# Optimization experiments

Hardware: AMD Instinct MI355X
Metric: run time of the kernel (lower is better)

Reference implementation:

```python
import jax, jax.numpy as jnp
import numpy as np
from jax.scipy.special import logsumexp

G, E, K, D, B, L, M, KN = 32000, 256, 8, 6, 4, 512, 64, 4
STEP, EPS = 0.05, 1.0


def setup_inputs() -> dict:
    key = jax.random.key(0)
    ks = jax.random.split(key, 16)
    s = 0.05  # weight scale for numerical stability
    return {
        'masked': jax.random.randint(ks[0], (B, L), 0, G),
        'unmasked': jax.random.randint(ks[1], (B, L), 0, G),
        'mask': jax.random.randint(ks[2], (B, M), 0, L),
        'summer': jnp.ones((B, M), jnp.float32),
        'embed': jax.random.normal(ks[3], (G, E), jnp.float32) * s,
        'pos': jax.random.normal(ks[4], (L, E), jnp.float32) * s,
        'Wt': jax.random.normal(ks[5], (D, E, E), jnp.float32) * s,
        'Wc': jax.random.normal(ks[6], (D, E, E), jnp.float32) * s,
        'Wq': jax.random.normal(ks[7], (D, K * E, E), jnp.float32) * s,
        'Wd': jax.random.normal(ks[8], (D, K * E, K * E), jnp.float32) * s,
        'Wo': jax.random.normal(ks[9], (D, K * E, E), jnp.float32) * s,
        'Wkc': jax.random.normal(ks[10], (E * KN, E), jnp.float32) * s,
        'bkc': jax.random.normal(ks[11], (E * KN,), jnp.float32) * s,
        'Wem': jax.random.normal(ks[12], (E, E), jnp.float32) * s,
    }


def _norm(x):
    # y / (eps + y.std(-1, unbiased)); torch std is ddof=1
    return x / (EPS + jnp.std(x, axis=-1, ddof=1, keepdims=True))


def reference(masked, unmasked, mask, summer, embed, pos, Wt, Wc, Wq, Wd, Wo, Wkc, bkc, Wem):
    b, l = masked.shape
    # batch init: token + positional embedding, normalized
    xsa = _norm(embed[masked] + pos[None, :l])  # (B,L,E)
    inv_sqrt_e = 1.0 / (E ** 0.5)
    for d in range(D):
        # local transition terms (roll +/- 1 along sequence)
        xsad = jax.nn.relu(jnp.roll(xsa, 1, axis=1) @ Wt[d]) @ Wc[d]
        xsad = xsad + jax.nn.relu(jnp.roll(xsa, -1, axis=1) @ Wc[d].T) @ Wt[d].T
        # QKV_Attention: K query heads against raw xsa keys/values
        q = (xsa @ Wq[d].T).reshape(b, l, K, E)           # (B,L,K,E)
        hijk = jnp.einsum('blke,bme->blkm', q, xsa) * inv_sqrt_e  # (B,L,K,L)
        pijk = jax.nn.softmax(hijk, axis=-1)
        yik = jnp.einsum('blkm,bme->blke', pijk, xsa)      # (B,L,K,E)
        xid = yik.reshape(b, l, K * E)
        # Dense -> ReLU -> Dense (mode 1)
        xidact = jax.nn.relu(xid @ Wd[d].T)                # (B,L,K*E)
        xsad = xsad + xidact @ Wo[d]                       # (B,L,E)
        # gradnorm + residual update + layernorm
        xsad = _norm(xsad)
        xsa = _norm(xsa + STEP * xsad)
    # loss head: gather masked positions
    lptok = jnp.take_along_axis(xsa, mask[:, :, None], axis=1)  # (B,M,E)
    m = mask.shape[1]
    xx = (lptok @ Wkc.T + bkc).reshape(b, m * KN, E)       # kchoice
    xx = jnp.einsum('bne,ble->bnl', xx, xsa)               # (B,M*KN,L)
    xx = jnp.einsum('bnl,ble->bne', xx, xsa)               # (B,M*KN,E)
    logits = (xx @ Wem) @ embed.T                          # (B,M*KN,G)
    k_lp = jax.nn.log_softmax(logits, axis=-1).reshape(b, m, KN, G)
    lp = logsumexp(k_lp, axis=-2) - jnp.float32(np.log(KN))  # (B,M,G)
    tgt = jnp.take_along_axis(unmasked, mask, axis=1)       # (B,M)
    cent = jnp.take_along_axis(lp, tgt[:, :, None], axis=-1)[:, :, 0]
    loss = -(cent * summer).sum(-1) / jnp.clip(summer.sum(-1), 1.0, None)
    return loss
```

## Files before the change

### kernel.cpp

```cpp
#include <hip/hip_runtime.h>
#include <math.h>
#include <stdint.h>

#define G_ 32000
#define E_ 256
#define K_ 8
#define D_ 6
#define B_ 4
#define L_ 512
#define M_ 64
#define KN_ 4
#define STEP_ 0.05f
#define BL_ (B_ * L_)
#define KE_ (K_ * E_)
#define NSPLIT_ 50
#define GCH_ 10

typedef __attribute__((ext_vector_type(8))) short short8;
typedef __attribute__((ext_vector_type(4))) float f32x4;
typedef __attribute__((ext_vector_type(4))) short short4v;

__device__ __forceinline__ short f2bf(float f) {
  unsigned u = __builtin_bit_cast(unsigned, f);
  unsigned r = (u + 0x7fffu + ((u >> 16) & 1u)) >> 16;
  return (short)r;
}
__device__ __forceinline__ float bf2f(short h) {
  return __builtin_bit_cast(float, ((unsigned)(unsigned short)h) << 16);
}

__device__ __forceinline__ void gload16(const void* g, void* l) {
  __builtin_amdgcn_global_load_lds(
      reinterpret_cast<const __attribute__((address_space(1))) void*>(
          reinterpret_cast<uintptr_t>(g)),
      reinterpret_cast<__attribute__((address_space(3))) void*>(
          reinterpret_cast<uintptr_t>(l)),
      16, 0, 0);
}

__device__ __forceinline__ float wsum(float v) {
#pragma unroll
  for (int o = 32; o > 0; o >>= 1) v += __shfl_xor(v, o, 64);
  return v;
}
__device__ __forceinline__ float block_sum(float v, float* sm) {
  v = wsum(v);
  int wid = threadIdx.x >> 6, lane = threadIdx.x & 63;
  if (lane == 0) sm[wid] = v;
  __syncthreads();
  float r = sm[0] + sm[1] + sm[2] + sm[3];
  __syncthreads();
  return r;
}

template <bool RELU, bool OBF>
__global__ __launch_bounds__(256) void mg128x64_k(
    const short* __restrict__ A, const short* __restrict__ B,
    void* __restrict__ Cg, int Kd, int lda, int ldb, int ldc) {
  __shared__ short As[128 * 64];
  __shared__ short Bs[64 * 64];
  int m0 = blockIdx.y * 128, n0 = blockIdx.x * 64;
  int t = threadIdx.x, w = t >> 6, l = t & 63;
  int l16 = l & 15, qd = l >> 4, hi8 = qd * 8;
  int wr_ = w >> 1, wc_ = w & 1;
  int sr = l >> 3;
  int scol = ((l & 7) * 8) ^ (sr << 3);
  f32x4 acc[4][2];
#pragma unroll
  for (int i = 0; i < 4; i++)
#pragma unroll
    for (int j = 0; j < 2; j++) acc[i][j] = {0.f, 0.f, 0.f, 0.f};

  for (int k0 = 0; k0 < Kd; k0 += 64) {
    __syncthreads();
#pragma unroll
    for (int c = 0; c < 4; c++) {
      int sub = w * 4 + c;
      int r = sub * 8 + sr;
      gload16(A + (long)(m0 + r) * lda + k0 + scol, &As[sub * 512]);
    }
#pragma unroll
    for (int c = 0; c < 2; c++) {
      int sub = w * 2 + c;
      int r = sub * 8 + sr;
      gload16(B + (long)(n0 + r) * ldb + k0 + scol, &Bs[sub * 512]);
    }
    __syncthreads();
#pragma unroll
    for (int ks = 0; ks < 2; ks++) {
      short8 af[4], bf[2];
#pragma unroll
      for (int rf = 0; rf < 4; rf++) {
        int row = wr_ * 64 + rf * 16 + l16;
        af[rf] = *(const short8*)&As[(row * 64 + ks * 32 + hi8) ^ ((row & 7) << 3)];
      }
#pragma unroll
      for (int cf = 0; cf < 2; cf++) {
        int row = wc_ * 32 + cf * 16 + l16;
        bf[cf] = *(const short8*)&Bs[(row * 64 + ks * 32 + hi8) ^ ((row & 7) << 3)];
      }
#pragma unroll
      for (int rf = 0; rf < 4; rf++)
#pragma unroll
        for (int cf = 0; cf < 2; cf++)
          acc[rf][cf] = __builtin_amdgcn_mfma_f32_16x16x32_bf16(
              af[rf], bf[cf], acc[rf][cf], 0, 0, 0);
    }
  }
#pragma unroll
  for (int rf = 0; rf < 4; rf++) {
#pragma unroll
    for (int cf = 0; cf < 2; cf++) {
      int col = n0 + wc_ * 32 + cf * 16 + l16;
#pragma unroll
      for (int j = 0; j < 4; j++) {
        int row = m0 + wr_ * 64 + rf * 16 + qd * 4 + j;
        float v = acc[rf][cf][j];
        if (RELU) v = fmaxf(v, 0.f);
        long idx = (long)row * ldc + col;
        if (OBF) ((short*)Cg)[idx] = f2bf(v);
        else ((float*)Cg)[idx] = v;
      }
    }
  }
}

__global__ __launch_bounds__(256) void mg64sk_k(
    const short* __restrict__ A, const short* __restrict__ B,
    float* __restrict__ P, int Klen, int lda, int ldb, int ldc, long pstride) {
  __shared__ short As[64 * 64];
  __shared__ short Bs[64 * 64];
  int z = blockIdx.z;
  int kbase = z * Klen;
  int m0 = blockIdx.y * 64, n0 = blockIdx.x * 64;
  int t = threadIdx.x, w = t >> 6, l = t & 63;
  int l16 = l & 15, qd = l >> 4, hi8 = qd * 8;
  int wr_ = w >> 1, wc_ = w & 1;
  int sr = l >> 3;
  int scol = ((l & 7) * 8) ^ (sr << 3);
  f32x4 acc[2][2];
#pragma unroll
  for (int i = 0; i < 2; i++)
#pragma unroll
    for (int j = 0; j < 2; j++) acc[i][j] = {0.f, 0.f, 0.f, 0.f};

  for (int k0 = 0; k0 < Klen; k0 += 64) {
    __syncthreads();
#pragma unroll
    for (int c = 0; c < 2; c++) {
      int sub = w * 2 + c;
      int r = sub * 8 + sr;
      gload16(A + (long)(m0 + r) * lda + kbase + k0 + scol, &As[sub * 512]);
      gload16(B + (long)(n0 + r) * ldb + kbase + k0 + scol, &Bs[sub * 512]);
    }
    __syncthreads();
#pragma unroll
    for (int ks = 0; ks < 2; ks++) {
      short8 af[2], bf[2];
#pragma unroll
      for (int rf = 0; rf < 2; rf++) {
        int row = wr_ * 32 + rf * 16 + l16;
        af[rf] = *(const short8*)&As[(row * 64 + ks * 32 + hi8) ^ ((row & 7) << 3)];
      }
#pragma unroll
      for (int cf = 0; cf < 2; cf++) {
        int row = wc_ * 32 + cf * 16 + l16;
        bf[cf] = *(const short8*)&Bs[(row * 64 + ks * 32 + hi8) ^ ((row & 7) << 3)];
      }
#pragma unroll
      for (int rf = 0; rf < 2; rf++)
#pragma unroll
        for (int cf = 0; cf < 2; cf++)
          acc[rf][cf] = __builtin_amdgcn_mfma_f32_16x16x32_bf16(
              af[rf], bf[cf], acc[rf][cf], 0, 0, 0);
    }
  }
  float* Pz = P + z * pstride;
#pragma unroll
  for (int rf = 0; rf < 2; rf++) {
#pragma unroll
    for (int cf = 0; cf < 2; cf++) {
      int col = n0 + wc_ * 32 + cf * 16 + l16;
#pragma unroll
      for (int j = 0; j < 4; j++) {
        int row = m0 + wr_ * 32 + rf * 16 + qd * 4 + j;
        Pz[(long)row * ldc + col] = acc[rf][cf][j];
      }
    }
  }
}

template <bool BIAS>
__global__ __launch_bounds__(256) void mgh_k(
    const short* __restrict__ Ag, const short* __restrict__ Bg,
    short* __restrict__ Cg, const float* __restrict__ bias, int Kd, int lda,
    int ldb, int ldc, long sA, long sB, long sC) {
  __shared__ short As[64 * 64];
  __shared__ short Bs[64 * 64];
  int z = blockIdx.z;
  const short* A = Ag + z * sA;
  const short* B = Bg + z * sB;
  short* C = Cg + z * sC;
  int m0 = blockIdx.y * 64, n0 = blockIdx.x * 64;
  int t = threadIdx.x, w = t >> 6, l = t & 63;
  int l16 = l & 15, qd = l >> 4, hi8 = qd * 8;
  int wr_ = w >> 1, wc_ = w & 1;
  int sr = l >> 3;
  int scol = ((l & 7) * 8) ^ (sr << 3);
  f32x4 acc[2][2];
#pragma unroll
  for (int i = 0; i < 2; i++)
#pragma unroll
    for (int j = 0; j < 2; j++) acc[i][j] = {0.f, 0.f, 0.f, 0.f};

  for (int k0 = 0; k0 < Kd; k0 += 64) {
    __syncthreads();
#pragma unroll
    for (int c = 0; c < 2; c++) {
      int sub = w * 2 + c;
      int r = sub * 8 + sr;
      gload16(A + (long)(m0 + r) * lda + k0 + scol, &As[sub * 512]);
      gload16(B + (long)(n0 + r) * ldb + k0 + scol, &Bs[sub * 512]);
    }
    __syncthreads();
#pragma unroll
    for (int ks = 0; ks < 2; ks++) {
      short8 af[2], bf[2];
#pragma unroll
      for (int rf = 0; rf < 2; rf++) {
        int row = wr_ * 32 + rf * 16 + l16;
        af[rf] = *(const short8*)&As[(row * 64 + ks * 32 + hi8) ^ ((row & 7) << 3)];
      }
#pragma unroll
      for (int cf = 0; cf < 2; cf++) {
        int row = wc_ * 32 + cf * 16 + l16;
        bf[cf] = *(const short8*)&Bs[(row * 64 + ks * 32 + hi8) ^ ((row & 7) << 3)];
      }
#pragma unroll
      for (int rf = 0; rf < 2; rf++)
#pragma unroll
        for (int cf = 0; cf < 2; cf++)
          acc[rf][cf] = __builtin_amdgcn_mfma_f32_16x16x32_bf16(
              af[rf], bf[cf], acc[rf][cf], 0, 0, 0);
    }
  }
#pragma unroll
  for (int rf = 0; rf < 2; rf++) {
#pragma unroll
    for (int cf = 0; cf < 2; cf++) {
      int col = n0 + wc_ * 32 + cf * 16 + l16;
      float bv = BIAS ? bias[col] : 0.f;
#pragma unroll
      for (int j = 0; j < 4; j++) {
        int row = m0 + wr_ * 32 + rf * 16 + qd * 4 + j;
        C[(long)row * ldc + col] = f2bf(acc[rf][cf][j] + bv);
      }
    }
  }
}

__global__ __launch_bounds__(256) void tpair_k(
    const short* __restrict__ xsa_bf, const short* __restrict__ wtT,
    const short* __restrict__ wcb, short* __restrict__ T) {
  __shared__ short As[64 * 64];
  __shared__ short Bs[64 * 64];
  int z = blockIdx.z;
  const short* Bb = z ? wcb : wtT;
  int rollv = z ? -1 : 1;
  int m0 = blockIdx.y * 64, n0 = blockIdx.x * 64;
  int t = threadIdx.x, w = t >> 6, l = t & 63;
  int l16 = l & 15, qd = l >> 4, hi8 = qd * 8;
  int wr_ = w >> 1, wc_ = w & 1;
  int sr = l >> 3;
  int scol = ((l & 7) * 8) ^ (sr << 3);
  f32x4 acc[2][2];
#pragma unroll
  for (int i = 0; i < 2; i++)
#pragma unroll
    for (int j = 0; j < 2; j++) acc[i][j] = {0.f, 0.f, 0.f, 0.f};
  for (int k0 = 0; k0 < E_; k0 += 64) {
    __syncthreads();
#pragma unroll
    for (int c = 0; c < 2; c++) {
      int sub = w * 2 + c;
      int r = sub * 8 + sr;
      int gr = m0 + r;
      int bb = gr >> 9, pp = gr & (L_ - 1);
      gr = (bb << 9) | ((pp - rollv + L_) & (L_ - 1));
      gload16(xsa_bf + (long)gr * E_ + k0 + scol, &As[sub * 512]);
      gload16(Bb + (long)(n0 + r) * E_ + k0 + scol, &Bs[sub * 512]);
    }
    __syncthreads();
#pragma unroll
    for (int ks = 0; ks < 2; ks++) {
      short8 af[2], bf[2];
#pragma unroll
      for (int rf = 0; rf < 2; rf++) {
        int row = wr_ * 32 + rf * 16 + l16;
        af[rf] = *(const short8*)&As[(row * 64 + ks * 32 + hi8) ^ ((row & 7) << 3)];
      }
#pragma unroll
      for (int cf = 0; cf < 2; cf++) {
        int row = wc_ * 32 + cf * 16 + l16;
        bf[cf] = *(const short8*)&Bs[(row * 64 + ks * 32 + hi8) ^ ((row & 7) << 3)];
      }
#pragma unroll
      for (int rf = 0; rf < 2; rf++)
#pragma unroll
        for (int cf = 0; cf < 2; cf++)
          acc[rf][cf] = __builtin_amdgcn_mfma_f32_16x16x32_bf16(
              af[rf], bf[cf], acc[rf][cf], 0, 0, 0);
    }
  }
#pragma unroll
  for (int rf = 0; rf < 2; rf++) {
#pragma unroll
    for (int cf = 0; cf < 2; cf++) {
      int col = n0 + wc_ * 32 + cf * 16 + l16;
#pragma unroll
      for (int j = 0; j < 4; j++) {
        int row = m0 + wr_ * 32 + rf * 16 + qd * 4 + j;
        T[(long)row * 512 + z * 256 + col] = f2bf(fmaxf(acc[rf][cf][j], 0.f));
      }
    }
  }
}

__global__ __launch_bounds__(512, 2) void flash3_k(
    const short* __restrict__ q_bf, const short* __restrict__ xsa_bf,
    const short* __restrict__ xsaT_bf, short* __restrict__ y_bf) {
  __shared__ short smem[69888];
  float* Obuf = (float*)smem;
  float* mst = (float*)&smem[69632];
  float* lst = mst + 64;
  int q0 = blockIdx.x * 64, hk = blockIdx.y, b = blockIdx.z;
  int t = threadIdx.x, w = t >> 6, l = t & 63;
  int l16 = l & 15, qd = l >> 4, hi8 = qd * 8;
  int qb = w & 3, half = w >> 2;
  const float scale = 0.0625f;

  short8 qf[8];
  {
    const short* qrow =
        q_bf + (long)(b * L_ + q0 + qb * 16 + l16) * KE_ + hk * 256;
#pragma unroll
    for (int ks = 0; ks < 8; ks++)
      qf[ks] = *(const short8*)(qrow + ks * 32 + hi8);
  }
  f32x4 acc_o[16];
#pragma unroll
  for (int i = 0; i < 16; i++) acc_o[i] = {0.f, 0.f, 0.f, 0.f};
  float mreg[4], lreg[4];
#pragma unroll
  for (int j = 0; j < 4; j++) { mreg[j] = -1e30f; lreg[j] = 0.f; }

  auto STAGE = [&](int nbuf, int it) {
#pragma unroll
    for (int c = 0; c < 4; c++) {
      int ch = w * 4 + c, hh = ch >> 4, rp = ch & 15;
      int row = rp * 2 + (l >> 5);
      int colsw = ((l & 31) * 8) ^ ((row & 7) << 3);
      gload16(xsa_bf + (long)(b * L_ + hh * 256 + it * 32 + row) * E_ + colsw,
              &smem[(nbuf * 2 + hh) * 8192 + rp * 512]);
    }
#pragma unroll
    for (int c = 0; c < 4; c++) {
      int ch = w * 4 + c, hh = ch >> 4, rg = ch & 15;
      int er = rg * 16 + (l >> 2);
      int col = (l & 3) * 8;
      gload16(xsaT_bf + (long)(b * E_ + er) * L_ + hh * 256 + it * 32 + col,
              &smem[32768 + (nbuf * 2 + hh) * 8192 + rg * 512]);
    }
  };

  STAGE(0, 0);
  __syncthreads();
  int cur = 0;
  for (int it = 0; it < 8; it++) {
    if (it < 7) STAGE(cur ^ 1, it + 1);
    const short* Kb = &smem[(cur * 2 + half) * 8192];
    const short* Vb = &smem[32768 + (cur * 2 + half) * 8192];
    short* Pw = &smem[65536 + w * 512];
    f32x4 s4[2];
    s4[0] = {0.f, 0.f, 0.f, 0.f};
    s4[1] = {0.f, 0.f, 0.f, 0.f};
#pragma unroll
    for (int ks = 0; ks < 8; ks++) {
#pragma unroll
      for (int cf = 0; cf < 2; cf++) {
        int row = cf * 16 + l16;
        short8 kb = *(const short8*)&Kb[row * 256 +
                                        ((ks * 32 + hi8) ^ ((row & 7) << 3))];
        s4[cf] = __builtin_amdgcn_mfma_f32_16x16x32_bf16(qf[ks], kb, s4[cf], 0, 0, 0);
      }
    }
    float alpha[4];
#pragma unroll
    for (int j = 0; j < 4; j++) {
      float v0 = s4[0][j] * scale, v1 = s4[1][j] * scale;
      float rmax = fmaxf(v0, v1);
#pragma unroll
      for (int mk = 1; mk <= 8; mk <<= 1) rmax = fmaxf(rmax, __shfl_xor(rmax, mk, 64));
      float mn = fmaxf(mreg[j], rmax);
      float p0 = __expf(v0 - mn), p1 = __expf(v1 - mn);
      float ps = p0 + p1;
#pragma unroll
      for (int mk = 1; mk <= 8; mk <<= 1) ps += __shfl_xor(ps, mk, 64);
      alpha[j] = __expf(mreg[j] - mn);
      lreg[j] = lreg[j] * alpha[j] + ps;
      mreg[j] = mn;
      int r = qd * 4 + j;
      Pw[r * 32 + l16] = f2bf(p0);
      Pw[r * 32 + 16 + l16] = f2bf(p1);
    }
#pragma unroll
    for (int cfo = 0; cfo < 16; cfo++)
#pragma unroll
      for (int j = 0; j < 4; j++) acc_o[cfo][j] *= alpha[j];
    short8 pa = *(const short8*)&Pw[l16 * 32 + hi8];
#pragma unroll
    for (int cfo = 0; cfo < 16; cfo++) {
      int er = cfo * 16 + l16;
      short8 vb = *(const short8*)&Vb[er * 32 + hi8];
      acc_o[cfo] = __builtin_amdgcn_mfma_f32_16x16x32_bf16(pa, vb, acc_o[cfo], 0, 0, 0);
    }
    __syncthreads();
    cur ^= 1;
  }
  if (half == 1) {
#pragma unroll
    for (int cfo = 0; cfo < 16; cfo++)
#pragma unroll
      for (int j = 0; j < 4; j++)
        Obuf[qb * 4096 + (qd * 4 + j) * 256 + cfo * 16 + l16] = acc_o[cfo][j];
    if (l16 == 0) {
#pragma unroll
      for (int j = 0; j < 4; j++) {
        mst[qb * 16 + qd * 4 + j] = mreg[j];
        lst[qb * 16 + qd * 4 + j] = lreg[j];
      }
    }
  }
  __syncthreads();
  if (half == 0) {
#pragma unroll
    for (int j = 0; j < 4; j++) {
      int r = qd * 4 + j;
      float m1 = mst[qb * 16 + r], l1 = lst[qb * 16 + r];
      float mn = fmaxf(mreg[j], m1);
      float a0 = __expf(mreg[j] - mn), a1 = __expf(m1 - mn);
      float linv = 1.0f / (lreg[j] * a0 + l1 * a1);
      short* yrow = y_bf + (long)(b * L_ + q0 + qb * 16 + r) * KE_ + hk * 256;
#pragma unroll
      for (int cfo = 0; cfo < 16; cfo++) {
        float o1 = Obuf[qb * 4096 + r * 256 + cfo * 16 + l16];
        yrow[cfo * 16 + l16] = f2bf((acc_o[cfo][j] * a0 + o1 * a1) * linv);
      }
    }
  }
}

__global__ __launch_bounds__(256) void finish_k(
    const float* __restrict__ Ptr, const float* __restrict__ Pwo,
    float* __restrict__ xsa, short* __restrict__ xsa_bf,
    short* __restrict__ xsaT_bf) {
  long r = blockIdx.x;
  int b = (int)(r / L_), ll = (int)(r % L_);
  int t = threadIdx.x;
  __shared__ float sm[4];
  long off = r * E_ + t;
  const long ps = (long)BL_ * E_;
  float vd = Ptr[off] + Ptr[ps + off] + Pwo[off] + Pwo[ps + off] +
             Pwo[2 * ps + off] + Pwo[3 * ps + off];
  float s1 = block_sum(vd, sm);
  float s2 = block_sum(vd * vd, sm);
  float mean = s1 * (1.0f / E_);
  float var = (s2 - s1 * mean) * (1.0f / (E_ - 1));
  float vdn = vd / (1.0f + sqrtf(fmaxf(var, 0.f)));
  float u = xsa[off] + STEP_ * vdn;
  s1 = block_sum(u, sm);
  s2 = block_sum(u * u, sm);
  mean = s1 * (1.0f / E_);
  var = (s2 - s1 * mean) * (1.0f / (E_ - 1));
  float xn = u / (1.0f + sqrtf(fmaxf(var, 0.f)));
  xsa[off] = xn;
  short h = f2bf(xn);
  xsa_bf[off] = h;
  xsaT_bf[((long)b * E_ + t) * L_ + ll] = h;
}

__global__ __launch_bounds__(256) void lse2_k(
    const short* __restrict__ tmat_bf, const short* __restrict__ embed_bf,
    float* __restrict__ mpart, float* __restrict__ spart) {
  __shared__ short Bs[64 * 256];
  int split = blockIdx.x, rb = blockIdx.y;
  int t = threadIdx.x, w = t >> 6, l = t & 63;
  int l16 = l & 15, qd = l >> 4, hi8 = qd * 8;
  short8 areg[8];
  {
    const short* ar = tmat_bf + (long)(rb * 64 + w * 16 + l16) * E_;
#pragma unroll
    for (int ks = 0; ks < 8; ks++) areg[ks] = *(const short8*)(ar + ks * 32 + hi8);
  }
  float m[4], s[4];
#pragma unroll
  for (int j = 0; j < 4; j++) { m[j] = -1e30f; s[j] = 0.f; }
  long gbase = (long)split * (GCH_ * 64);
  for (int ch = 0; ch < GCH_; ch++) {
    long g0 = gbase + ch * 64;
    __syncthreads();
#pragma unroll
    for (int j = 0; j < 8; j++) {
      int sub = w * 8 + j;
      int r = sub * 2 + (l >> 5);
      int col = ((l & 31) * 8) ^ ((r & 7) << 3);
      gload16(embed_bf + (g0 + r) * E_ + col, &Bs[sub * 512]);
    }
    __syncthreads();
    f32x4 acc[4];
#pragma unroll
    for (int cf = 0; cf < 4; cf++) acc[cf] = {0.f, 0.f, 0.f, 0.f};
#pragma unroll
    for (int ks = 0; ks < 8; ks++) {
#pragma unroll
      for (int cf = 0; cf < 4; cf++) {
        int row = cf * 16 + l16;
        short8 b = *(const short8*)&Bs[(row * 256 + ks * 32 + hi8) ^ ((row & 7) << 3)];
        acc[cf] = __builtin_amdgcn_mfma_f32_16x16x32_bf16(areg[ks], b, acc[cf], 0, 0, 0);
      }
    }
#pragma unroll
    for (int j = 0; j < 4; j++) {
      float vm = fmaxf(fmaxf(acc[0][j], acc[1][j]), fmaxf(acc[2][j], acc[3][j]));
      float mn = fmaxf(m[j], vm);
      s[j] = s[j] * __expf(m[j] - mn) + __expf(acc[0][j] - mn) +
             __expf(acc[1][j] - mn) + __expf(acc[2][j] - mn) +
             __expf(acc[3][j] - mn);
      m[j] = mn;
    }
  }
#pragma unroll
  for (int j = 0; j < 4; j++) {
#pragma unroll
    for (int mask = 1; mask <= 8; mask <<= 1) {
      float mo = __shfl_xor(m[j], mask, 64);
      float so = __shfl_xor(s[j], mask, 64);
      float mn = fmaxf(m[j], mo);
      s[j] = s[j] * __expf(m[j] - mn) + so * __expf(mo - mn);
      m[j] = mn;
    }
    if (l16 == 0) {
      int row = rb * 64 + w * 16 + qd * 4 + j;
      mpart[(long)row * NSPLIT_ + split] = m[j];
      spart[(long)row * NSPLIT_ + split] = s[j];
    }
  }
}

__device__ __forceinline__ void cvt8_blk(const float* __restrict__ src,
                                         short* __restrict__ dst, int blk, int t) {
  long i = (long)blk * 256 + t;
  const float4* s4 = (const float4*)src;
  float4 a = s4[2 * i], b = s4[2 * i + 1];
  short8 o = {f2bf(a.x), f2bf(a.y), f2bf(a.z), f2bf(a.w),
              f2bf(b.x), f2bf(b.y), f2bf(b.z), f2bf(b.w)};
  ((short8*)dst)[i] = o;
}
__device__ __forceinline__ void trans_blk(const float* __restrict__ src,
                                          short* __restrict__ dst, int bx, int by,
                                          int C, int ldd, float (*tile)[33], int t) {
  int c0 = bx * 32, r0 = by * 32;
  int tx = t & 31, ty = t >> 5;
#pragma unroll
  for (int k = 0; k < 4; k++)
    tile[ty + k * 8][tx] = src[(long)(r0 + ty + k * 8) * C + c0 + tx];
  __syncthreads();
#pragma unroll
  for (int k = 0; k < 4; k++)
    dst[(long)(c0 + ty + k * 8) * ldd + r0 + tx] = f2bf(tile[tx][ty + k * 8]);
}
#define WCVT_BLKS (4000 + 128 + 6 * 2368 + 64 + 6 * 640)
__global__ __launch_bounds__(256) void wcvt_all_k(
    const float* __restrict__ embed, const float* __restrict__ Wt,
    const float* __restrict__ Wc, const float* __restrict__ Wq,
    const float* __restrict__ Wd, const float* __restrict__ Wo,
    const float* __restrict__ Wkc, const float* __restrict__ Wem,
    short* embed_bf, short* wcb, short* wq, short* wd, short* wtT, short* woT,
    short* wcat, short* wkc_bf, short* wemT) {
  __shared__ float tile[32][33];
  int blk = blockIdx.x, t = threadIdx.x;
  if (blk < 4000) { cvt8_blk(embed, embed_bf, blk, t); return; }
  blk -= 4000;
  if (blk < 128) { cvt8_blk(Wkc, wkc_bf, blk, t); return; }
  blk -= 128;
  if (blk < 6 * 2368) {
    int d = blk / 2368;
    int r = blk - d * 2368;
    if (r < 2048) { cvt8_blk(Wd + (long)d * KE_ * KE_, wd + (long)d * KE_ * KE_, r, t); return; }
    r -= 2048;
    if (r < 256) { cvt8_blk(Wq + (long)d * KE_ * E_, wq + (long)d * KE_ * E_, r, t); return; }
    r -= 256;
    if (r < 32) { cvt8_blk(Wc + (long)d * E_ * E_, wcb + (long)d * E_ * E_, r, t); return; }
    r -= 32;
    {
      const float* Wt_d = Wt + (long)d * E_ * E_;
      short* wcat_d = wcat + (long)d * E_ * 512;
      long i = (long)r * 256 + t;
      int n = (int)(i >> 5);
      int kc = (int)(i & 31) * 8;
      float4 a = *(const float4*)(Wt_d + (long)n * E_ + kc);
      float4 b = *(const float4*)(Wt_d + (long)n * E_ + kc + 4);
      short8 o = {f2bf(a.x), f2bf(a.y), f2bf(a.z), f2bf(a.w),
                  f2bf(b.x), f2bf(b.y), f2bf(b.z), f2bf(b.w)};
      *(short8*)(wcat_d + (long)n * 512 + 256 + kc) = o;
      return;
    }
  }
  blk -= 6 * 2368;
  if (blk < 64) { trans_blk(Wem, wemT, blk & 7, blk >> 3, E_, E_, tile, t); return; }
  blk -= 64;
  {
    int d = blk / 640;
    int r = blk - d * 640;
    if (r < 64) {
      trans_blk(Wt + (long)d * E_ * E_, wtT + (long)d * E_ * E_, r & 7, r >> 3,
                E_, E_, tile, t);
      return;
    }
    r -= 64;
    if (r < 512) {
      trans_blk(Wo + (long)d * KE_ * E_, woT + (long)d * E_ * KE_, r & 7, r >> 3,
                E_, KE_, tile, t);
      return;
    }
    r -= 512;
    trans_blk(Wc + (long)d * E_ * E_, wcat + (long)d * E_ * 512, r & 7, r >> 3,
              E_, 512, tile, t);
  }
}

__global__ __launch_bounds__(256) void embed_init_k(
    const int* __restrict__ masked, const float* __restrict__ embed,
    const float* __restrict__ pos, float* __restrict__ xsa,
    short* __restrict__ xsa_bf, short* __restrict__ xsaT_bf) {
  int bl = blockIdx.x;
  int b = bl / L_, ll = bl % L_;
  int t = threadIdx.x;
  __shared__ float sm[4];
  int tok = masked[bl];
  float v = embed[(long)tok * E_ + t] + pos[(long)ll * E_ + t];
  float s1 = block_sum(v, sm);
  float s2 = block_sum(v * v, sm);
  float mean = s1 * (1.0f / E_);
  float var = (s2 - s1 * mean) * (1.0f / (E_ - 1));
  float xn = v / (1.0f + sqrtf(fmaxf(var, 0.f)));
  xsa[(long)bl * E_ + t] = xn;
  short h = f2bf(xn);
  xsa_bf[(long)bl * E_ + t] = h;
  xsaT_bf[((long)b * E_ + t) * L_ + ll] = h;
}

__global__ __launch_bounds__(256) void gatherbf_k(const short* __restrict__ xsa_bf,
                                                  const int* __restrict__ mask,
                                                  short* __restrict__ lptok_bf) {
  int bm = blockIdx.x;
  int b = bm >> 6;
  int t = threadIdx.x;
  int p = mask[bm];
  lptok_bf[(long)bm * E_ + t] = xsa_bf[((long)b * L_ + p) * E_ + t];
}

__global__ __launch_bounds__(256) void cent_k(
    const short* __restrict__ tmat_bf, const float* __restrict__ embed,
    const int* __restrict__ mask, const int* __restrict__ unmasked,
    const float* __restrict__ mpart, const float* __restrict__ spart,
    float* __restrict__ cent) {
  int bm = blockIdx.x;
  int b = bm >> 6, m = bm & 63;
  int t = threadIdx.x;
  __shared__ float sm[4];
  __shared__ float tlv[KN_];
  int pos = mask[bm];
  int tgt = unmasked[b * L_ + pos];
  float ev = embed[(long)tgt * E_ + t];
  for (int kn = 0; kn < KN_; kn++) {
    long grow = (long)b * (M_ * KN_) + m * KN_ + kn;
    float tv = bf2f(tmat_bf[grow * E_ + t]);
    float dot = block_sum(tv * ev, sm);
    if (t == 0) {
      float M = -1e30f, S = 0.f;
      for (int i = 0; i < NSPLIT_; i++) {
        float m2 = mpart[grow * NSPLIT_ + i], s2 = spart[grow * NSPLIT_ + i];
        float MM = fmaxf(M, m2);
        S = S * __expf(M - MM) + s2 * __expf(m2 - MM);
        M = MM;
      }
      tlv[kn] = dot - (M + __logf(S));
    }
  }
  __syncthreads();
  if (t == 0) {
    float mx = fmaxf(fmaxf(tlv[0], tlv[1]), fmaxf(tlv[2], tlv[3]));
    float s = __expf(tlv[0] - mx) + __expf(tlv[1] - mx) + __expf(tlv[2] - mx) +
              __expf(tlv[3] - mx);
    cent[bm] = __logf(s) + mx - 1.3862943611198906f;
  }
}

__global__ __launch_bounds__(256) void loss_k(const float* __restrict__ cent,
                                              const float* __restrict__ summer,
                                              float* __restrict__ out) {
  int t = threadIdx.x;
  int b = t >> 6, m = t & 63;
  float c = cent[b * 64 + m], su = summer[b * 64 + m];
  float num = wsum(c * su);
  float den = wsum(su);
  if (m == 0) out[b] = -num / fmaxf(den, 1.0f);
}

extern "C" void kernel_launch(void* const* d_in, const int* in_sizes, int n_in,
                              void* d_out, int out_size, void* d_ws,
                              size_t ws_size, hipStream_t stream) {
  (void)in_sizes; (void)n_in; (void)out_size; (void)ws_size;
  const int* masked = (const int*)d_in[0];
  const int* unmasked = (const int*)d_in[1];
  const int* mask = (const int*)d_in[2];
  const float* summer = (const float*)d_in[3];
  const float* embed = (const float*)d_in[4];
  const float* pos = (const float*)d_in[5];
  const float* Wt = (const float*)d_in[6];
  const float* Wc = (const float*)d_in[7];
  const float* Wq = (const float*)d_in[8];
  const float* Wd = (const float*)d_in[9];
  const float* Wo = (const float*)d_in[10];
  const float* Wkc = (const float*)d_in[11];
  const float* bkc = (const float*)d_in[12];
  const float* Wem = (const float*)d_in[13];
  float* out = (float*)d_out;

  char* p = (char*)d_ws;
  auto take = [&](size_t bytes) {
    char* r = p;
    p += (bytes + 255) & ~(size_t)255;
    return r;
  };
  float* xsa = (float*)take((size_t)BL_ * E_ * 4);
  short* xsa_bf = (short*)take((size_t)BL_ * E_ * 2);
  short* xsaT_bf = (short*)take((size_t)BL_ * E_ * 2);
  short* t_buf = (short*)take((size_t)BL_ * 512 * 2);
  short* q_bf = (short*)take((size_t)BL_ * KE_ * 2);
  short* y_bf = (short*)take((size_t)BL_ * KE_ * 2);
  float* P_tr = (float*)take((size_t)2 * BL_ * E_ * 4);
  float* P_wo = (float*)take((size_t)4 * BL_ * E_ * 4);
  short* wcb = (short*)take((size_t)D_ * E_ * E_ * 2);
  short* wtT = (short*)take((size_t)D_ * E_ * E_ * 2);
  short* wq = (short*)take((size_t)D_ * KE_ * E_ * 2);
  short* wd = (short*)take((size_t)D_ * KE_ * KE_ * 2);
  short* woT = (short*)take((size_t)D_ * E_ * KE_ * 2);
  short* wcat = (short*)take((size_t)D_ * E_ * 512 * 2);
  short* wkc_bf = (short*)take((size_t)KN_ * E_ * E_ * 2);
  short* wemT = (short*)take((size_t)E_ * E_ * 2);
  short* embed_bf = (short*)take((size_t)G_ * E_ * 2);
  short* lptok_bf = (short*)take((size_t)B_ * M_ * E_ * 2);
  short* xx1_bf = (short*)take((size_t)B_ * M_ * KN_ * E_ * 2);
  short* xx2_bf = (short*)take((size_t)B_ * M_ * KN_ * L_ * 2);
  short* xx3_bf = (short*)take((size_t)B_ * M_ * KN_ * E_ * 2);
  short* tmat_bf = (short*)take((size_t)B_ * M_ * KN_ * E_ * 2);
  float* mpart = (float*)take((size_t)1024 * NSPLIT_ * 4);
  float* spart = (float*)take((size_t)1024 * NSPLIT_ * 4);
  float* cent = (float*)take((size_t)B_ * M_ * 4);

  dim3 blk(256);
  wcvt_all_k<<<WCVT_BLKS, blk, 0, stream>>>(embed, Wt, Wc, Wq, Wd, Wo, Wkc, Wem,
                                            embed_bf, wcb, wq, wd, wtT, woT,
                                            wcat, wkc_bf, wemT);
  embed_init_k<<<BL_, blk, 0, stream>>>(masked, embed, pos, xsa, xsa_bf, xsaT_bf);

  for (int d = 0; d < D_; d++) {
    short* wcb_d = wcb + (long)d * E_ * E_;
    short* wtT_d = wtT + (long)d * E_ * E_;
    short* wq_d = wq + (long)d * KE_ * E_;
    short* wd_d = wd + (long)d * KE_ * KE_;
    short* woT_d = woT + (long)d * E_ * KE_;
    short* wcat_d = wcat + (long)d * E_ * 512;

    tpair_k<<<dim3(4, 32, 2), blk, 0, stream>>>(xsa_bf, wtT_d, wcb_d, t_buf);
    mg64sk_k<<<dim3(4, 32, 2), blk, 0, stream>>>(t_buf, wcat_d, P_tr, 256, 512,
                                                 512, E_, (long)BL_ * E_);
    mg128x64_k<false, true><<<dim3(32, 16), blk, 0, stream>>>(
        xsa_bf, wq_d, q_bf, E_, E_, E_, KE_);
    flash3_k<<<dim3(L_ / 64, K_, B_), dim3(512), 0, stream>>>(q_bf, xsa_bf,
                                                              xsaT_bf, y_bf);
    mg128x64_k<true, true><<<dim3(32, 16), blk, 0, stream>>>(
        y_bf, wd_d, q_bf, KE_, KE_, KE_, KE_);
    mg64sk_k<<<dim3(4, 32, 4), blk, 0, stream>>>(q_bf, woT_d, P_wo, 512, KE_,
                                                 KE_, E_, (long)BL_ * E_);
    finish_k<<<BL_, blk, 0, stream>>>(P_tr, P_wo, xsa, xsa_bf, xsaT_bf);
  }

  gatherbf_k<<<B_ * M_, blk, 0, stream>>>(xsa_bf, mask, lptok_bf);
  mgh_k<true><<<dim3(16, 4, 1), blk, 0, stream>>>(
      lptok_bf, wkc_bf, xx1_bf, bkc, E_, E_, E_, KN_ * E_, 0, 0, 0);
  mgh_k<false><<<dim3(8, 4, B_), blk, 0, stream>>>(
      xx1_bf, xsa_bf, xx2_bf, nullptr, E_, E_, E_, L_,
      (long)M_ * KN_ * E_, (long)L_ * E_, (long)M_ * KN_ * L_);
  mgh_k<false><<<dim3(4, 4, B_), blk, 0, stream>>>(
      xx2_bf, xsaT_bf, xx3_bf, nullptr, L_, L_, L_, E_,
      (long)M_ * KN_ * L_, (long)E_ * L_, (long)M_ * KN_ * E_);
  mgh_k<false><<<dim3(4, 16, 1), blk, 0, stream>>>(
      xx3_bf, wemT, tmat_bf, nullptr, E_, E_, E_, E_, 0, 0, 0);
  lse2_k<<<dim3(NSPLIT_, 16), blk, 0, stream>>>(tmat_bf, embed_bf, mpart, spart);
  cent_k<<<B_ * M_, blk, 0, stream>>>(tmat_bf, embed, mask, unmasked, mpart,
                                      spart, cent);
  loss_k<<<1, blk, 0, stream>>>(cent, summer, out);
}
```

Before: 686.1 us.

## Double vocab splits, parallelize split merge, add MFMA priority, widen transposes

Doubles the number of vocabulary splits in the logits/logsumexp kernel (half the chunks per block) to raise parallelism. The per-row merge of split partials in cent_k moves from a serial single-thread loop to block-wide max and sum reductions. s_setprio hints are placed around the MFMA loops in the attention and logits kernels, and the weight-transpose conversion switches to 64x64 bf16 tiles with vectorized loads and stores. These are several unrelated tweaks; the added splits double the partial writes, and the new reductions add barriers per kn iteration.

Result: no change. 677.1 us (-1.3%).

```diff
diff --git a/kernel.cpp b/kernel.cpp
--- a/kernel.cpp
+++ b/kernel.cpp
@@ -13,8 +13,8 @@
 #define STEP_ 0.05f
 #define BL_ (B_ * L_)
 #define KE_ (K_ * E_)
-#define NSPLIT_ 50
-#define GCH_ 10
+#define NSPLIT_ 100
+#define GCH_ 5
 
 typedef __attribute__((ext_vector_type(8))) short short8;
 typedef __attribute__((ext_vector_type(4))) float f32x4;
@@ -43,12 +43,26 @@
   for (int o = 32; o > 0; o >>= 1) v += __shfl_xor(v, o, 64);
   return v;
 }
+__device__ __forceinline__ float wmaxr(float v) {
+#pragma unroll
+  for (int o = 32; o > 0; o >>= 1) v = fmaxf(v, __shfl_xor(v, o, 64));
+  return v;
+}
 __device__ __forceinline__ float block_sum(float v, float* sm) {
   v = wsum(v);
   int wid = threadIdx.x >> 6, lane = threadIdx.x & 63;
   if (lane == 0) sm[wid] = v;
   __syncthreads();
   float r = sm[0] + sm[1] + sm[2] + sm[3];
+  __syncthreads();
+  return r;
+}
+__device__ __forceinline__ float block_max(float v, float* sm) {
+  v = wmaxr(v);
+  int wid = threadIdx.x >> 6, lane = threadIdx.x & 63;
+  if (lane == 0) sm[wid] = v;
+  __syncthreads();
+  float r = fmaxf(fmaxf(sm[0], sm[1]), fmaxf(sm[2], sm[3]));
   __syncthreads();
   return r;
 }
@@ -384,6 +398,7 @@
     f32x4 s4[2];
     s4[0] = {0.f, 0.f, 0.f, 0.f};
     s4[1] = {0.f, 0.f, 0.f, 0.f};
+    __builtin_amdgcn_s_setprio(1);
 #pragma unroll
     for (int ks = 0; ks < 8; ks++) {
 #pragma unroll
@@ -394,6 +409,7 @@
         s4[cf] = __builtin_amdgcn_mfma_f32_16x16x32_bf16(qf[ks], kb, s4[cf], 0, 0, 0);
       }
     }
+    __builtin_amdgcn_s_setprio(0);
     float alpha[4];
 #pragma unroll
     for (int j = 0; j < 4; j++) {
@@ -418,12 +434,14 @@
 #pragma unroll
       for (int j = 0; j < 4; j++) acc_o[cfo][j] *= alpha[j];
     short8 pa = *(const short8*)&Pw[l16 * 32 + hi8];
+    __builtin_amdgcn_s_setprio(1);
 #pragma unroll
     for (int cfo = 0; cfo < 16; cfo++) {
       int er = cfo * 16 + l16;
       short8 vb = *(const short8*)&Vb[er * 32 + hi8];
       acc_o[cfo] = __builtin_amdgcn_mfma_f32_16x16x32_bf16(pa, vb, acc_o[cfo], 0, 0, 0);
     }
+    __builtin_amdgcn_s_setprio(0);
     __syncthreads();
     cur ^= 1;
   }
@@ -520,6 +538,7 @@
     f32x4 acc[4];
 #pragma unroll
     for (int cf = 0; cf < 4; cf++) acc[cf] = {0.f, 0.f, 0.f, 0.f};
+    __builtin_amdgcn_s_setprio(1);
 #pragma unroll
     for (int ks = 0; ks < 8; ks++) {
 #pragma unroll
@@ -529,6 +548,7 @@
         acc[cf] = __builtin_amdgcn_mfma_f32_16x16x32_bf16(areg[ks], b, acc[cf], 0, 0, 0);
       }
     }
+    __builtin_amdgcn_s_setprio(0);
 #pragma unroll
     for (int j = 0; j < 4; j++) {
       float vm = fmaxf(fmaxf(acc[0][j], acc[1][j]), fmaxf(acc[2][j], acc[3][j]));
@@ -566,20 +586,35 @@
               f2bf(b.x), f2bf(b.y), f2bf(b.z), f2bf(b.w)};
   ((short8*)dst)[i] = o;
 }
-__device__ __forceinline__ void trans_blk(const float* __restrict__ src,
-                                          short* __restrict__ dst, int bx, int by,
-                                          int C, int ldd, float (*tile)[33], int t) {
-  int c0 = bx * 32, r0 = by * 32;
-  int tx = t & 31, ty = t >> 5;
-#pragma unroll
-  for (int k = 0; k < 4; k++)
-    tile[ty + k * 8][tx] = src[(long)(r0 + ty + k * 8) * C + c0 + tx];
+__device__ __forceinline__ void trans64_blk(const float* __restrict__ src,
+                                            short* __restrict__ dst, int bx,
+                                            int by, int C, int ldd,
+                                            short (*tile)[68], int t) {
+  int c0 = bx * 64, r0 = by * 64;
+  int tr = t >> 4;
+  int tc = (t & 15) * 4;
+#pragma unroll
+  for (int k = 0; k < 4; k++) {
+    int r = tr + k * 16;
+    float4 v = *(const float4*)(src + (long)(r0 + r) * C + c0 + tc);
+    tile[r][tc + 0] = f2bf(v.x);
+    tile[r][tc + 1] = f2bf(v.y);
+    tile[r][tc + 2] = f2bf(v.z);
+    tile[r][tc + 3] = f2bf(v.w);
+  }
   __syncthreads();
 #pragma unroll
-  for (int k = 0; k < 4; k++)
-    dst[(long)(c0 + ty + k * 8) * ldd + r0 + tx] = f2bf(tile[tx][ty + k * 8]);
-}
-#define WCVT_BLKS (4000 + 128 + 6 * 2368 + 64 + 6 * 640)
+  for (int j = 0; j < 2; j++) {
+    int ch = t + j * 256;
+    int rd = ch >> 3;
+    int cd = (ch & 7) * 8;
+    short8 o;
+#pragma unroll
+    for (int e = 0; e < 8; e++) o[e] = tile[cd + e][rd];
+    *(short8*)(dst + (long)(c0 + rd) * ldd + r0 + cd) = o;
+  }
+}
+#define WCVT_BLKS (4000 + 128 + 6 * 2368 + 16 + 6 * 160)
 __global__ __launch_bounds__(256) void wcvt_all_k(
     const float* __restrict__ embed, const float* __restrict__ Wt,
     const float* __restrict__ Wc, const float* __restrict__ Wq,
@@ -587,7 +622,7 @@
     const float* __restrict__ Wkc, const float* __restrict__ Wem,
     short* embed_bf, short* wcb, short* wq, short* wd, short* wtT, short* woT,
     short* wcat, short* wkc_bf, short* wemT) {
-  __shared__ float tile[32][33];
+  __shared__ short tile[64][68];
   int blk = blockIdx.x, t = threadIdx.x;
   if (blk < 4000) { cvt8_blk(embed, embed_bf, blk, t); return; }
   blk -= 4000;
@@ -617,25 +652,25 @@
     }
   }
   blk -= 6 * 2368;
-  if (blk < 64) { trans_blk(Wem, wemT, blk & 7, blk >> 3, E_, E_, tile, t); return; }
-  blk -= 64;
+  if (blk < 16) { trans64_blk(Wem, wemT, blk & 3, blk >> 2, E_, E_, tile, t); return; }
+  blk -= 16;
   {
-    int d = blk / 640;
-    int r = blk - d * 640;
-    if (r < 64) {
-      trans_blk(Wt + (long)d * E_ * E_, wtT + (long)d * E_ * E_, r & 7, r >> 3,
-                E_, E_, tile, t);
+    int d = blk / 160;
+    int r = blk - d * 160;
+    if (r < 16) {
+      trans64_blk(Wt + (long)d * E_ * E_, wtT + (long)d * E_ * E_, r & 3,
+                  r >> 2, E_, E_, tile, t);
       return;
     }
-    r -= 64;
-    if (r < 512) {
-      trans_blk(Wo + (long)d * KE_ * E_, woT + (long)d * E_ * KE_, r & 7, r >> 3,
-                E_, KE_, tile, t);
+    r -= 16;
+    if (r < 128) {
+      trans64_blk(Wo + (long)d * KE_ * E_, woT + (long)d * E_ * KE_, r & 3,
+                  r >> 2, E_, KE_, tile, t);
       return;
     }
-    r -= 512;
-    trans_blk(Wc + (long)d * E_ * E_, wcat + (long)d * E_ * 512, r & 7, r >> 3,
-              E_, 512, tile, t);
+    r -= 128;
+    trans64_blk(Wc + (long)d * E_ * E_, wcat + (long)d * E_ * 512, r & 3,
+                r >> 2, E_, 512, tile, t);
   }
 }
 
@@ -687,16 +722,11 @@
     long grow = (long)b * (M_ * KN_) + m * KN_ + kn;
     float tv = bf2f(tmat_bf[grow * E_ + t]);
     float dot = block_sum(tv * ev, sm);
-    if (t == 0) {
-      float M = -1e30f, S = 0.f;
-      for (int i = 0; i < NSPLIT_; i++) {
-        float m2 = mpart[grow * NSPLIT_ + i], s2 = spart[grow * NSPLIT_ + i];
-        float MM = fmaxf(M, m2);
-        S = S * __expf(M - MM) + s2 * __expf(m2 - MM);
-        M = MM;
-      }
-      tlv[kn] = dot - (M + __logf(S));
-    }
+    float m2 = (t < NSPLIT_) ? mpart[grow * NSPLIT_ + t] : -1e30f;
+    float s2 = (t < NSPLIT_) ? spart[grow * NSPLIT_ + t] : 0.f;
+    float Mx = block_max(m2, sm);
+    float S = block_sum(s2 * __expf(m2 - Mx), sm);
+    if (t == 0) tlv[kn] = dot - (Mx + __logf(S));
   }
   __syncthreads();
   if (t == 0) {
```
